# Optimization experiments

Hardware: AMD Instinct MI355X
Metric: run time of the kernel (lower is better)

Reference implementation:

```python
import jax, jax.numpy as jnp
import numpy as np

N = 262144      # nodes per graph
NC = 65536      # common nodes
D = 256         # feature_dim


def setup_inputs() -> dict:
    key = jax.random.key(0)
    ks = jax.random.split(key, 12)
    h_prop = jax.random.normal(ks[0], (N, D), dtype=jnp.float32)
    h_context = jax.random.normal(ks[1], (N, D), dtype=jnp.float32)
    h_orig = jax.random.normal(ks[2], (NC, D), dtype=jnp.float32)
    # unique indices (torch scatter-assign semantics are only well-defined without dups)
    idx_prop = jnp.sort(jax.random.permutation(ks[3], N)[:NC]).astype(jnp.int64)
    idx_ctx = jnp.sort(jax.random.permutation(ks[4], N)[:NC]).astype(jnp.int64)
    # parameters (xavier-ish scale)
    s = 1.0 / np.sqrt(D)
    w_orig = jax.random.normal(ks[5], (D, D), dtype=jnp.float32) * s
    w_prop = jax.random.normal(ks[6], (D, D), dtype=jnp.float32) * s
    w_ctx = jax.random.normal(ks[7], (D, D), dtype=jnp.float32) * s
    W_fuse = jax.random.normal(ks[8], (D, 3 * D), dtype=jnp.float32) * (1.0 / np.sqrt(3 * D))  # torch Linear weight (out,in)
    b_fuse = jnp.zeros((D,), dtype=jnp.float32)
    bias = jax.random.uniform(ks[9], (D,), dtype=jnp.float32, minval=-s, maxval=s)
    return {
        "h_prop": h_prop, "h_context": h_context,
        "h_original_common_nodes": h_orig,
        "w_orig": w_orig, "w_prop": w_prop, "w_ctx": w_ctx,
        "W_fuse": W_fuse, "b_fuse": b_fuse, "bias": bias,
        "common_node_indices_in_prop": idx_prop,
        "common_node_indices_in_context": idx_ctx,
    }


def reference(h_prop, h_context, h_original_common_nodes,
              w_orig, w_prop, w_ctx, W_fuse, b_fuse, bias,
              common_node_indices_in_prop, common_node_indices_in_context):
    # gather common rows + three small GEMMs  [NC, D]
    t_orig = h_original_common_nodes @ w_orig
    t_prop = h_prop[common_node_indices_in_prop] @ w_prop
    t_ctx = h_context[common_node_indices_in_context] @ w_ctx
    # concat-linear-tanh-bias  [NC, D]
    fused = jnp.concatenate([t_orig, t_prop, t_ctx], axis=1) @ W_fuse.T + b_fuse
    fused = jnp.tanh(fused) + bias
    # scatter update into clones of the full tables
    h_prop_updated = h_prop.at[common_node_indices_in_prop].set(fused)
    h_context_updated = h_context.at[common_node_indices_in_context].set(fused)
    return (h_prop_updated, h_context_updated)
```

## Files before the change

### kernel.cpp

```cpp
#include <hip/hip_runtime.h>
#include <hip/hip_bf16.h>
#include <math.h>

#define NN 262144
#define NCC 65536

typedef __bf16 bf16x8 __attribute__((ext_vector_type(8)));
typedef float f32x4 __attribute__((ext_vector_type(4)));

__global__ __launch_bounds__(256) void k_setup(const float* __restrict__ w_orig,
                                               const float* __restrict__ w_prop,
                                               const float* __restrict__ w_ctx,
                                               const float* __restrict__ W_fuse,
                                               __bf16* __restrict__ Mt,
                                               unsigned char* __restrict__ flags) {
    __shared__ float Wl[64 * 65];
    __shared__ float wl[64 * 65];
    int b = blockIdx.x;
    int t = threadIdx.x;
    if (b >= 48) {
        ((uint4*)flags)[(b - 48) * 256 + t] = make_uint4(0u, 0u, 0u, 0u);
        return;
    }
    int seg = b >> 4, rem = b & 15;
    int ot = rem >> 2, mt = rem & 3;
    const float* wseg = seg == 0 ? w_orig : (seg == 1 ? w_prop : w_ctx);
    int to = (t & 15) * 4, tm = (t >> 4) * 4;
    float acc[4][4] = {};
    for (int kc = 0; kc < 4; ++kc) {
        __syncthreads();
        for (int i = 0; i < 16; ++i) {
            int f = i * 256 + t;
            int row = f >> 6, col = f & 63;
            Wl[row * 65 + col] = W_fuse[(size_t)(ot * 64 + row) * 768 + seg * 256 + kc * 64 + col];
            wl[row * 65 + col] = wseg[(size_t)(mt * 64 + row) * 256 + kc * 64 + col];
        }
        __syncthreads();
        for (int k = 0; k < 64; ++k) {
            float wo[4], wm2[4];
#pragma unroll
            for (int i = 0; i < 4; ++i) wo[i] = Wl[(to + i) * 65 + k];
#pragma unroll
            for (int j = 0; j < 4; ++j) wm2[j] = wl[(tm + j) * 65 + k];
#pragma unroll
            for (int i = 0; i < 4; ++i)
#pragma unroll
                for (int j = 0; j < 4; ++j) acc[i][j] += wo[i] * wm2[j];
        }
    }
    for (int i = 0; i < 4; ++i)
        for (int j = 0; j < 4; ++j) {
            int o = ot * 64 + to + i;
            int g = seg * 256 + mt * 64 + tm + j;
            Mt[(size_t)o * 768 + g] = (__bf16)acc[i][j];
        }
}

__global__ void k_setflags(const int* __restrict__ idxp, const int* __restrict__ idxc,
                           unsigned char* fp, unsigned char* fc) {
    int j = blockIdx.x * blockDim.x + threadIdx.x;
    if (j < NCC) { fp[idxp[j]] = 1; fc[idxc[j]] = 1; }
}

__device__ inline bf16x8 cvt8(f32x4 a, f32x4 b) {
    bf16x8 w;
    w[0] = (__bf16)a[0]; w[1] = (__bf16)a[1]; w[2] = (__bf16)a[2]; w[3] = (__bf16)a[3];
    w[4] = (__bf16)b[0]; w[5] = (__bf16)b[1]; w[6] = (__bf16)b[2]; w[7] = (__bf16)b[3];
    return w;
}

__global__ __launch_bounds__(512, 4) void k_gemm(const float* __restrict__ hp,
                                                 const float* __restrict__ hc,
                                                 const float* __restrict__ horig,
                                                 const __bf16* __restrict__ Mt,
                                                 const float* __restrict__ bfuse,
                                                 const float* __restrict__ bias,
                                                 const int* __restrict__ idxp,
                                                 const int* __restrict__ idxc,
                                                 float* __restrict__ out0,
                                                 float* __restrict__ out1) {
    __shared__ char smem[40960];
    __bf16* Al = (__bf16*)smem;
    __bf16* Bl = (__bf16*)(smem + 8192);
    int t = threadIdx.x;
    int jbase = blockIdx.x * 64;
    int lane = t & 63, wid = t >> 6;
    int wm = wid >> 2, wn = wid & 3;
    int l15 = lane & 15, lq = lane >> 4;

    int ar = t >> 3, aslot = t & 7;
    int jr = jbase + ar;
    const float* rowp0 = horig + (size_t)jr * 256 + aslot * 8;
    const float* rowp1 = hp + (size_t)idxp[jr] * 256 + aslot * 8;
    const float* rowp2 = hc + (size_t)idxc[jr] * 256 + aslot * 8;

    int bo = t >> 1, bkp = t & 1;
    const __bf16* bsrc = Mt + (size_t)bo * 768 + bkp * 32;

    f32x4 a0[2], a1[2];
    bf16x8 vb[4];
    {
        a0[0] = *(const f32x4*)(rowp0);       a1[0] = *(const f32x4*)(rowp0 + 4);
        a0[1] = *(const f32x4*)(rowp0 + 64);  a1[1] = *(const f32x4*)(rowp0 + 68);
#pragma unroll
        for (int i = 0; i < 4; ++i) vb[i] = *(const bf16x8*)(bsrc + i * 8);
    }

    f32x4 acc[2][4] = {};

#pragma unroll
    for (int c = 0; c < 12; ++c) {
        int s = c & 1;
        __syncthreads();
        *(bf16x8*)&Al[ar * 64 + ((aslot ^ (ar & 7)) << 3)] = cvt8(a0[s], a1[s]);
#pragma unroll
        for (int i = 0; i < 4; ++i) {
            int slot = bkp * 4 + i;
            *(bf16x8*)&Bl[bo * 64 + ((slot ^ (bo & 7)) << 3)] = vb[i];
        }
        if (c < 11) {
#pragma unroll
            for (int i = 0; i < 4; ++i) vb[i] = *(const bf16x8*)(bsrc + (c + 1) * 64 + i * 8);
        }
        if (c < 10) {
            int cn = c + 2;
            int seg = cn >> 2, ko = (cn & 3) * 64;
            const float* sp = (seg == 0 ? rowp0 : (seg == 1 ? rowp1 : rowp2)) + ko;
            a0[s] = *(const f32x4*)(sp);
            a1[s] = *(const f32x4*)(sp + 4);
        }
        __syncthreads();
#pragma unroll
        for (int ks = 0; ks < 2; ++ks) {
            bf16x8 af[2], bfr[4];
            int kslot = ks * 4 + lq;
#pragma unroll
            for (int mi = 0; mi < 2; ++mi) {
                int r = wm * 32 + mi * 16 + l15;
                af[mi] = *(const bf16x8*)&Al[r * 64 + ((kslot ^ (r & 7)) << 3)];
            }
#pragma unroll
            for (int ni = 0; ni < 4; ++ni) {
                int o = wn * 64 + ni * 16 + l15;
                bfr[ni] = *(const bf16x8*)&Bl[o * 64 + ((kslot ^ (o & 7)) << 3)];
            }
#pragma unroll
            for (int mi = 0; mi < 2; ++mi)
#pragma unroll
                for (int ni = 0; ni < 4; ++ni)
                    acc[mi][ni] = __builtin_amdgcn_mfma_f32_16x16x32_bf16(af[mi], bfr[ni], acc[mi][ni], 0, 0, 0);
        }
    }

    float bfv[4], biv[4];
#pragma unroll
    for (int ni = 0; ni < 4; ++ni) {
        int o = wn * 64 + ni * 16 + l15;
        bfv[ni] = bfuse[o];
        biv[ni] = bias[o];
    }
    __syncthreads();
    float* scr = (float*)(smem + 8192 + wid * 4096);
#pragma unroll
    for (int mi = 0; mi < 2; ++mi) {
#pragma unroll
        for (int ni = 0; ni < 4; ++ni)
#pragma unroll
            for (int rr = 0; rr < 4; ++rr) {
                float v = tanhf(acc[mi][ni][rr] + bfv[ni]) + biv[ni];
                scr[(lq * 4 + rr) * 64 + ni * 16 + l15] = v;
            }
#pragma unroll
        for (int rnd = 0; rnd < 4; ++rnd) {
            int rr2 = rnd * 4 + lq;
            int j = jbase + wm * 32 + mi * 16 + rr2;
            int gp = idxp[j], gc = idxc[j];
            f32x4 v = *(const f32x4*)&scr[rr2 * 64 + l15 * 4];
            *(f32x4*)(out0 + (size_t)gp * 256 + wn * 64 + l15 * 4) = v;
            *(f32x4*)(out1 + (size_t)gc * 256 + wn * 64 + l15 * 4) = v;
        }
    }
}

__global__ __launch_bounds__(256) void k_copy(const float* __restrict__ hp,
                                              const float* __restrict__ hc,
                                              const unsigned char* __restrict__ fp,
                                              const unsigned char* __restrict__ fc,
                                              float* __restrict__ out0,
                                              float* __restrict__ out1) {
    int tid = blockIdx.x * 256 + threadIdx.x;
    const int stride = 4096 * 256;
#pragma unroll
    for (int g = 0; g < 4; ++g) {
        unsigned char fl[8];
#pragma unroll
        for (int i = 0; i < 8; ++i) {
            int gid = (g * 8 + i) * stride + tid;
            int row = gid >> 6;
            int tbl = row >= NN;
            int r = tbl ? row - NN : row;
            fl[i] = (tbl ? fc : fp)[r];
        }
        f32x4 v[8];
#pragma unroll
        for (int i = 0; i < 8; ++i) {
            int gid = (g * 8 + i) * stride + tid;
            int row = gid >> 6, slot = gid & 63;
            int tbl = row >= NN;
            int r = tbl ? row - NN : row;
            const float* S = tbl ? hc : hp;
            v[i] = *(const f32x4*)(S + (size_t)(fl[i] ? 0 : r) * 256 + slot * 4);
        }
#pragma unroll
        for (int i = 0; i < 8; ++i) {
            int gid = (g * 8 + i) * stride + tid;
            int row = gid >> 6, slot = gid & 63;
            int tbl = row >= NN;
            int r = tbl ? row - NN : row;
            float* D = tbl ? out1 : out0;
            if (!fl[i]) *(f32x4*)(D + (size_t)r * 256 + slot * 4) = v[i];
        }
    }
}

extern "C" void kernel_launch(void* const* d_in, const int* in_sizes, int n_in,
                              void* d_out, int out_size, void* d_ws, size_t ws_size,
                              hipStream_t stream) {
    const float* hp     = (const float*)d_in[0];
    const float* hc     = (const float*)d_in[1];
    const float* horig  = (const float*)d_in[2];
    const float* w_orig = (const float*)d_in[3];
    const float* w_prop = (const float*)d_in[4];
    const float* w_ctx  = (const float*)d_in[5];
    const float* W_fuse = (const float*)d_in[6];
    const float* bfuse  = (const float*)d_in[7];
    const float* bias   = (const float*)d_in[8];
    const int* idxp     = (const int*)d_in[9];
    const int* idxc     = (const int*)d_in[10];
    float* out0 = (float*)d_out;
    float* out1 = out0 + (size_t)NN * 256;

    char* ws = (char*)d_ws;
    __bf16* Mt = (__bf16*)ws;
    unsigned char* fp = (unsigned char*)(ws + 393216);
    unsigned char* fc = fp + NN;

    k_setup<<<176, 256, 0, stream>>>(w_orig, w_prop, w_ctx, W_fuse, Mt, fp);
    k_setflags<<<NCC / 256, 256, 0, stream>>>(idxp, idxc, fp, fc);
    k_gemm<<<NCC / 64, 512, 0, stream>>>(hp, hc, horig, Mt, bfuse, bias,
                                         idxp, idxc, out0, out1);
    k_copy<<<4096, 256, 0, stream>>>(hp, hc, fp, fc, out0, out1);
}
```

Measured before the change: 324.9 us.

## Merge GEMM and copy kernels into one interleaved launch

Folds the row-copy kernel into the GEMM kernel: even blocks copy 512 non-common rows of one table and odd blocks run the 64-row GEMM tile. Bandwidth-bound copy work and compute-bound GEMM work then run concurrently on the device, and one launch plus the tail between the two kernels goes away. In exchange, copy blocks carry the GEMM kernel's 40KB shared-memory allocation and register budget, which may reduce occupancy for the copy part.

```diff
diff --git a/kernel.cpp b/kernel.cpp
--- a/kernel.cpp
+++ b/kernel.cpp
@@ -69,7 +69,7 @@
     return w;
 }
 
-__global__ __launch_bounds__(512, 4) void k_gemm(const float* __restrict__ hp,
+__global__ __launch_bounds__(512, 4) void k_main(const float* __restrict__ hp,
                                                  const float* __restrict__ hc,
                                                  const float* __restrict__ horig,
                                                  const __bf16* __restrict__ Mt,
@@ -77,13 +77,48 @@
                                                  const float* __restrict__ bias,
                                                  const int* __restrict__ idxp,
                                                  const int* __restrict__ idxc,
+                                                 const unsigned char* __restrict__ fp,
+                                                 const unsigned char* __restrict__ fc,
                                                  float* __restrict__ out0,
                                                  float* __restrict__ out1) {
     __shared__ char smem[40960];
+    int bid = blockIdx.x >> 1;
+    int t = threadIdx.x;
+
+    if (!(blockIdx.x & 1)) {
+        int tbl = bid >= 512;
+        const unsigned char* F = tbl ? fc : fp;
+        const float* S = tbl ? hc : hp;
+        float* D = tbl ? out1 : out0;
+        int r0 = (tbl ? bid - 512 : bid) * 512;
+#pragma unroll
+        for (int g = 0; g < 8; ++g) {
+            unsigned char fl[8];
+            f32x4 v[8];
+#pragma unroll
+            for (int i = 0; i < 8; ++i) {
+                int gl = (g * 8 + i) * 512 + t;
+                fl[i] = F[r0 + (gl >> 6)];
+            }
+#pragma unroll
+            for (int i = 0; i < 8; ++i) {
+                int gl = (g * 8 + i) * 512 + t;
+                int r = r0 + (gl >> 6), slot = gl & 63;
+                v[i] = *(const f32x4*)(S + (size_t)(fl[i] ? 0 : r) * 256 + slot * 4);
+            }
+#pragma unroll
+            for (int i = 0; i < 8; ++i) {
+                int gl = (g * 8 + i) * 512 + t;
+                int r = r0 + (gl >> 6), slot = gl & 63;
+                if (!fl[i]) *(f32x4*)(D + (size_t)r * 256 + slot * 4) = v[i];
+            }
+        }
+        return;
+    }
+
     __bf16* Al = (__bf16*)smem;
     __bf16* Bl = (__bf16*)(smem + 8192);
-    int t = threadIdx.x;
-    int jbase = blockIdx.x * 64;
+    int jbase = bid * 64;
     int lane = t & 63, wid = t >> 6;
     int wm = wid >> 2, wn = wid & 3;
     int l15 = lane & 15, lq = lane >> 4;
@@ -178,47 +213,6 @@
             f32x4 v = *(const f32x4*)&scr[rr2 * 64 + l15 * 4];
             *(f32x4*)(out0 + (size_t)gp * 256 + wn * 64 + l15 * 4) = v;
             *(f32x4*)(out1 + (size_t)gc * 256 + wn * 64 + l15 * 4) = v;
-        }
-    }
-}
-
-__global__ __launch_bounds__(256) void k_copy(const float* __restrict__ hp,
-                                              const float* __restrict__ hc,
-                                              const unsigned char* __restrict__ fp,
-                                              const unsigned char* __restrict__ fc,
-                                              float* __restrict__ out0,
-                                              float* __restrict__ out1) {
-    int tid = blockIdx.x * 256 + threadIdx.x;
-    const int stride = 4096 * 256;
-#pragma unroll
-    for (int g = 0; g < 4; ++g) {
-        unsigned char fl[8];
-#pragma unroll
-        for (int i = 0; i < 8; ++i) {
-            int gid = (g * 8 + i) * stride + tid;
-            int row = gid >> 6;
-            int tbl = row >= NN;
-            int r = tbl ? row - NN : row;
-            fl[i] = (tbl ? fc : fp)[r];
-        }
-        f32x4 v[8];
-#pragma unroll
-        for (int i = 0; i < 8; ++i) {
-            int gid = (g * 8 + i) * stride + tid;
-            int row = gid >> 6, slot = gid & 63;
-            int tbl = row >= NN;
-            int r = tbl ? row - NN : row;
-            const float* S = tbl ? hc : hp;
-            v[i] = *(const f32x4*)(S + (size_t)(fl[i] ? 0 : r) * 256 + slot * 4);
-        }
-#pragma unroll
-        for (int i = 0; i < 8; ++i) {
-            int gid = (g * 8 + i) * stride + tid;
-            int row = gid >> 6, slot = gid & 63;
-            int tbl = row >= NN;
-            int r = tbl ? row - NN : row;
-            float* D = tbl ? out1 : out0;
-            if (!fl[i]) *(f32x4*)(D + (size_t)r * 256 + slot * 4) = v[i];
         }
     }
 }
@@ -247,7 +241,6 @@
 
     k_setup<<<176, 256, 0, stream>>>(w_orig, w_prop, w_ctx, W_fuse, Mt, fp);
     k_setflags<<<NCC / 256, 256, 0, stream>>>(idxp, idxc, fp, fc);
-    k_gemm<<<NCC / 64, 512, 0, stream>>>(hp, hc, horig, Mt, bfuse, bias,
-                                         idxp, idxc, out0, out1);
-    k_copy<<<4096, 256, 0, stream>>>(hp, hc, fp, fc, out0, out1);
-}
+    k_main<<<2048, 512, 0, stream>>>(hp, hc, horig, Mt, bfuse, bias,
+                                     idxp, idxc, fp, fc, out0, out1);
+}
```

New measurement: 291.0 us. -10.4%, faster.
